# Kernel optimization log

Hardware: AMD Instinct MI355X
Metric: run time of the kernel (lower is better)

The kernel has to match this reference:

```python
import jax, jax.numpy as jnp
import numpy as np

N, C, HW, HEADS = 2048, 16, 8, 4
F = C * HW * HW  # 1024
E = 16384
EPS = 1e-5
NEG_SLOPE = 0.2


def _bn(x, g, b):
    # training-mode BatchNorm2d over (N, H, W)
    m = x.mean(axis=(0, 2, 3), keepdims=True)
    v = x.var(axis=(0, 2, 3), keepdims=True)
    return (x - m) * jax.lax.rsqrt(v + EPS) * g[None, :, None, None] + b[None, :, None, None]


def _conv1x1(x, w, b):
    # 1x1 conv == per-pixel linear: w is [out_c, in_c]
    return jnp.einsum('nchw,oc->nohw', x, w) + b[None, :, None, None]


def _gatv2(xf, edge_index, wl, bl, wr, br, att, bias_gat):
    # xf: [N, F] node features
    xl = (xf @ wl + bl).reshape(N, HEADS, F)  # source-side transform (lin_l)
    xr = (xf @ wr + br).reshape(N, HEADS, F)  # target-side transform (lin_r)
    src, dst = edge_index[0], edge_index[1]
    loops = jnp.arange(N)
    # PyG default: remove existing self loops (mask them) then add self loops
    src_f = jnp.concatenate([src, loops])
    dst_f = jnp.concatenate([dst, loops])
    valid = jnp.concatenate([src != dst, jnp.ones((N,), bool)])
    xj = xl[src_f]                                   # [E+N, HEADS, F] gather
    e = jax.nn.leaky_relu(xj + xr[dst_f], negative_slope=NEG_SLOPE)
    logits = jnp.einsum('ehf,hf->eh', e, att)        # [E+N, HEADS]
    logits = jnp.where(valid[:, None], logits, -jnp.inf)
    mx = jax.lax.stop_gradient(jax.ops.segment_max(logits, dst_f, num_segments=N))
    expv = jnp.where(valid[:, None], jnp.exp(logits - mx[dst_f]), 0.0)
    denom = jax.ops.segment_sum(expv, dst_f, num_segments=N)
    alpha = expv / denom[dst_f]                      # segment softmax over incoming edges
    out = jax.ops.segment_sum(alpha[:, :, None] * xj, dst_f, num_segments=N)  # [N, HEADS, F]
    return out.reshape(N, HEADS * F) + bias_gat


def setup_inputs() -> dict:
    key = jax.random.key(0)
    ks = jax.random.split(key, 8)
    s = 0.02
    return {
        'x': jax.random.normal(ks[0], (N, C, HW, HW), jnp.float32),
        'edge_index': jax.random.randint(ks[1], (2, E), 0, N),
        'w1': jax.random.normal(ks[2], (C, C), jnp.float32) * s,
        'b1': jnp.zeros((C,), jnp.float32),
        'g1': jnp.ones((C,), jnp.float32),
        'be1': jnp.zeros((C,), jnp.float32),
        'wl': jax.random.normal(ks[3], (F, HEADS * F), jnp.float32) * s,
        'bl': jnp.zeros((HEADS * F,), jnp.float32),
        'wr': jax.random.normal(ks[4], (F, HEADS * F), jnp.float32) * s,
        'br': jnp.zeros((HEADS * F,), jnp.float32),
        'att': jax.random.normal(ks[5], (HEADS, F), jnp.float32) * s,
        'bias_gat': jnp.zeros((HEADS * F,), jnp.float32),
        'w2': jax.random.normal(ks[6], (C, HEADS * C), jnp.float32) * s,
        'b2': jnp.zeros((C,), jnp.float32),
        'g2': jnp.ones((C,), jnp.float32),
        'be2': jnp.zeros((C,), jnp.float32),
    }


def reference(x, edge_index, w1, b1, g1, be1, wl, bl, wr, br, att, bias_gat, w2, b2, g2, be2):
    res = x
    y = _bn(_conv1x1(x, w1, b1), g1, be1)            # fc1: Conv2d 1x1 + BN
    yf = y.reshape(N, F)
    g = _gatv2(yf, edge_index, wl, bl, wr, br, att, bias_gat)
    g = g.reshape(N, HEADS * C, HW, HW)
    out = _bn(_conv1x1(g, w2, b2), g2, be2)          # fc2: Conv2d 1x1 + BN
    return out + res                                  # DropPath(0.0) == Identity
```

## Files before the change

kernel.cpp:

```cpp
#include <hip/hip_runtime.h>
#include <stdint.h>

#define N_NODES 2048
#define F_DIM   1024
#define HEADS   4
#define NF      4096
#define ROW     8192
#define E_EDGES 16384
#define MAXE    (E_EDGES + N_NODES)
#define BN_EPS  1e-5f
#define NSLOPE  0.2f

typedef unsigned short ushort_t;
typedef __attribute__((ext_vector_type(8))) short bf16x8;
typedef __attribute__((ext_vector_type(4))) float f32x4;
typedef __attribute__((ext_vector_type(8))) unsigned short us8;

__device__ __forceinline__ float b2f(unsigned short u) {
    union { unsigned int i; float f; } x; x.i = ((unsigned int)u) << 16; return x.f;
}
__device__ __forceinline__ unsigned short f2b(float f) {
    union { float f; unsigned int i; } x; x.f = f;
    unsigned int r = x.i + 0x7fffu + ((x.i >> 16) & 1u);
    return (unsigned short)(r >> 16);
}
__device__ __forceinline__ ushort_t ld_canon(const void* src, size_t i, int f32) {
    return f32 ? f2b(((const float*)src)[i]) : ((const ushort_t*)src)[i];
}
__device__ __forceinline__ float ld_f(const void* src, size_t i, int f32) {
    return f32 ? ((const float*)src)[i] : b2f(((const ushort_t*)src)[i]);
}

__device__ __forceinline__ int sniff_f32_blk(const ushort_t* xu, int* lds_flag) {
    int t = threadIdx.x;
    if (t < 64) {
        unsigned e = (xu[2 * t] >> 7) & 0xFF;
        unsigned long long m = __ballot(e >= 0x90u);
        if (t == 0) *lds_flag = (__popcll(m) >= 3) ? 1 : 0;
    }
    __syncthreads();
    return *lds_flag;
}
__device__ __forceinline__ int sniff_i64_blk(const int* ei_raw, int* lds_flag) {
    int t = threadIdx.x;
    if (t < 64) {
        unsigned long long m = __ballot(ei_raw[2 * t + 1] != 0);
        if (t == 0) *lds_flag = (m == 0ull) ? 1 : 0;
    }
    __syncthreads();
    return *lds_flag;
}

__global__ __launch_bounds__(256) void k_prep(
    const void* __restrict__ wl, const void* __restrict__ wr,
    const int* __restrict__ ei_raw, const ushort_t* __restrict__ xu,
    const void* __restrict__ x, const void* __restrict__ w1, const void* __restrict__ b1,
    ushort_t* __restrict__ wT, int* __restrict__ counts,
    ushort_t* __restrict__ y0b, float* __restrict__ ps, float* __restrict__ pq)
{
    __shared__ ushort_t tl[64][65];
    __shared__ float xs[1024];
    __shared__ float sw[256];
    __shared__ float sb[16];
    __shared__ int sfl;
    int b = blockIdx.x, t = threadIdx.x;
    if (b < 2048) {
        int f32 = sniff_f32_blk(xu, &sfl);
        int z = b >> 10, rem = b & 1023;
        int bx = (rem & 63) * 64, by = (rem >> 6) * 64;
        const void* in = z ? wr : wl;
        ushort_t* outT = wT + (size_t)z * 4194304ull;
        #pragma unroll
        for (int i = 0; i < 16; ++i) {
            int idx = t + i * 256;
            int r = idx >> 6, c = idx & 63;
            tl[r][c] = ld_canon(in, (size_t)(by + r) * 4096 + bx + c, f32);
        }
        __syncthreads();
        #pragma unroll
        for (int i = 0; i < 16; ++i) {
            int idx = t + i * 256;
            int r = idx >> 6, c = idx & 63;
            outT[(size_t)(bx + r) * 1024 + by + c] = tl[c][r];
        }
    } else if (b < 2120) {
        int i64 = sniff_i64_blk(ei_raw, &sfl);
        int idx = (b - 2048) * 256 + t;
        if (idx < E_EDGES) {
            int s = i64 ? ei_raw[2 * idx] : ei_raw[idx];
            int d = i64 ? ei_raw[2 * (E_EDGES + idx)] : ei_raw[E_EDGES + idx];
            if (s != d) atomicAdd(&counts[d], 1);
        } else if (idx < MAXE) {
            atomicAdd(&counts[idx - E_EDGES], 1);
        }
    } else {
        int bid = b - 2120;
        int f32 = sniff_f32_blk(xu, &sfl);
        sw[t] = ld_f(w1, t, f32);
        if (t < 16) sb[t] = ld_f(b1, t, f32);
        int wave = t >> 6, lane = t & 63;
        float s[4] = {0,0,0,0}, q[4] = {0,0,0,0};
        for (int nn = 0; nn < 8; ++nn) {
            int n = bid * 8 + nn;
            __syncthreads();
            #pragma unroll
            for (int i = 0; i < 4; ++i) {
                int idx = t + i * 256;
                xs[idx] = ld_f(x, (size_t)n * 1024 + idx, f32);
            }
            __syncthreads();
            #pragma unroll
            for (int i = 0; i < 4; ++i) {
                int o = wave * 4 + i;
                float acc = sb[o];
                #pragma unroll
                for (int c = 0; c < 16; ++c) acc += xs[c * 64 + lane] * sw[o * 16 + c];
                y0b[(size_t)n * 1024 + o * 64 + lane] = f2b(acc);
                s[i] += acc; q[i] += acc * acc;
            }
        }
        #pragma unroll
        for (int i = 0; i < 4; ++i)
            for (int mm = 1; mm < 64; mm <<= 1) {
                s[i] += __shfl_xor(s[i], mm);
                q[i] += __shfl_xor(q[i], mm);
            }
        if (lane == 0)
            #pragma unroll
            for (int i = 0; i < 4; ++i) {
                ps[bid * 16 + wave * 4 + i] = s[i];
                pq[bid * 16 + wave * 4 + i] = q[i];
            }
    }
}

__global__ __launch_bounds__(256) void k_scatnorm(
    const int* __restrict__ ei_raw, const int* __restrict__ counts,
    int* __restrict__ cursor, int* __restrict__ offs, int* __restrict__ esrc,
    const ushort_t* __restrict__ y0b,
    const float* __restrict__ ps, const float* __restrict__ pq,
    const void* __restrict__ g1, const void* __restrict__ be1,
    const ushort_t* __restrict__ xu, ushort_t* __restrict__ xf)
{
    __shared__ int offl[2048];
    __shared__ int ts[256];
    __shared__ int sfl;
    __shared__ float red[2][64];
    __shared__ float scs[16], shs[16];
    int t = threadIdx.x;
    if (blockIdx.x < 72) {
        int i64 = sniff_i64_blk(ei_raw, &sfl);
        int loc[8]; int tot = 0;
        #pragma unroll
        for (int j = 0; j < 8; ++j) { loc[j] = counts[t * 8 + j]; tot += loc[j]; }
        ts[t] = tot; __syncthreads();
        for (int s = 1; s < 256; s <<= 1) {
            int v = (t >= s) ? ts[t - s] : 0;
            __syncthreads();
            ts[t] += v;
            __syncthreads();
        }
        int run = ts[t] - tot;
        #pragma unroll
        for (int j = 0; j < 8; ++j) { offl[t * 8 + j] = run; run += loc[j]; }
        __syncthreads();
        if (blockIdx.x == 0) {
            #pragma unroll
            for (int j = 0; j < 8; ++j) offs[t * 8 + j] = offl[t * 8 + j];
            if (t == 255) offs[2048] = run;
        }
        int idx = blockIdx.x * 256 + t;
        if (idx < E_EDGES) {
            int s = i64 ? ei_raw[2 * idx] : ei_raw[idx];
            int d = i64 ? ei_raw[2 * (E_EDGES + idx)] : ei_raw[E_EDGES + idx];
            if (s != d) esrc[offl[d] + atomicAdd(&cursor[d], 1)] = s;
        } else if (idx < MAXE) {
            int n = idx - E_EDGES;
            esrc[offl[n] + atomicAdd(&cursor[n], 1)] = n;
        }
    } else {
        int f32 = sniff_f32_blk(xu, &sfl);
        int lane = t & 63, wv = t >> 6;
        float s = 0.f, q = 0.f;
        #pragma unroll
        for (int i = 0; i < 16; ++i) { s += ps[i * 256 + t]; q += pq[i * 256 + t]; }
        s += __shfl_xor(s, 16); q += __shfl_xor(q, 16);
        s += __shfl_xor(s, 32); q += __shfl_xor(q, 32);
        if (lane < 16) { red[0][wv * 16 + lane] = s; red[1][wv * 16 + lane] = q; }
        __syncthreads();
        if (t < 16) {
            float S = red[0][t] + red[0][16 + t] + red[0][32 + t] + red[0][48 + t];
            float Q = red[1][t] + red[1][16 + t] + red[1][32 + t] + red[1][48 + t];
            const float inv = 1.0f / 131072.0f;
            float mean = S * inv;
            float var  = Q * inv - mean * mean;
            float sc = ld_f(g1, t, f32) * rsqrtf(var + BN_EPS);
            scs[t] = sc;
            shs[t] = ld_f(be1, t, f32) - mean * sc;
        }
        __syncthreads();
        size_t base = (size_t)(blockIdx.x - 72) * 4096 + t * 16;
        int ch = ((int)(base >> 6)) & 15;
        float sc = scs[ch], sh = shs[ch];
        us8 v0 = *(const us8*)(y0b + base), v1 = *(const us8*)(y0b + base + 8);
        us8 o0, o1;
        #pragma unroll
        for (int j = 0; j < 8; ++j) {
            o0[j] = f2b(b2f(v0[j]) * sc + sh);
            o1[j] = f2b(b2f(v1[j]) * sc + sh);
        }
        *(us8*)(xf + base) = o0;
        *(us8*)(xf + base + 8) = o1;
    }
}

__global__ __launch_bounds__(256) void k_gemm(
    const ushort_t* __restrict__ A, const ushort_t* __restrict__ BT,
    const void* __restrict__ blr, const void* __restrict__ brr,
    const ushort_t* __restrict__ xu, ushort_t* __restrict__ out)
{
    __shared__ __align__(16) ushort_t smem[16384];
    ushort_t* As0 = smem;
    ushort_t* As1 = smem + 4096;
    ushort_t* Bs0 = smem + 8192;
    ushort_t* Bs1 = smem + 12288;
    ushort_t* cs  = smem;
    __shared__ int sfl;
    int f32 = sniff_f32_blk(xu, &sfl);
    int tid = threadIdx.x;
    int wv = tid >> 6, ln = tid & 63;
    int m0 = blockIdx.y * 128, n0 = blockIdx.x * 128;
    int wm = (wv >> 1) * 64, wn = (wv & 1) * 64;
    int lr = ln & 15, quad = ln >> 4;

    f32x4 acc[4][4];
    #pragma unroll
    for (int i = 0; i < 4; ++i)
        #pragma unroll
        for (int j2 = 0; j2 < 4; ++j2) acc[i][j2] = (f32x4){0.f, 0.f, 0.f, 0.f};

    for (int k0 = 0; k0 < 1024; k0 += 64) {
        #pragma unroll
        for (int i = 0; i < 2; ++i) {
            int cbase = i * 256 + wv * 64;
            int ci = cbase + ln;
            int m = ci >> 2, kc = ci & 3;
            const ushort_t* ga = A + (size_t)(m0 + m) * 1024 + k0 + kc * 8;
            __builtin_amdgcn_global_load_lds(
                (const __attribute__((address_space(1))) void*)ga,
                (__attribute__((address_space(3))) void*)(&As0[cbase * 8]), 16, 0, 0);
            __builtin_amdgcn_global_load_lds(
                (const __attribute__((address_space(1))) void*)(ga + 32),
                (__attribute__((address_space(3))) void*)(&As1[cbase * 8]), 16, 0, 0);
            const ushort_t* gb = BT + (size_t)(n0 + m) * 1024 + k0 + kc * 8;
            __builtin_amdgcn_global_load_lds(
                (const __attribute__((address_space(1))) void*)gb,
                (__attribute__((address_space(3))) void*)(&Bs0[cbase * 8]), 16, 0, 0);
            __builtin_amdgcn_global_load_lds(
                (const __attribute__((address_space(1))) void*)(gb + 32),
                (__attribute__((address_space(3))) void*)(&Bs1[cbase * 8]), 16, 0, 0);
        }
        __syncthreads();
        #pragma unroll
        for (int p = 0; p < 2; ++p) {
            const ushort_t* Ap = p ? As1 : As0;
            const ushort_t* Bp = p ? Bs1 : Bs0;
            bf16x8 af[4], bfr[4];
            #pragma unroll
            for (int i = 0; i < 4; ++i)
                af[i] = *(const bf16x8*)(&Ap[(wm + i * 16 + lr) * 32 + quad * 8]);
            #pragma unroll
            for (int j2 = 0; j2 < 4; ++j2)
                bfr[j2] = *(const bf16x8*)(&Bp[(wn + j2 * 16 + lr) * 32 + quad * 8]);
            #pragma unroll
            for (int i = 0; i < 4; ++i)
                #pragma unroll
                for (int j2 = 0; j2 < 4; ++j2)
                    acc[i][j2] = __builtin_amdgcn_mfma_f32_16x16x32_bf16(af[i], bfr[j2], acc[i][j2], 0, 0, 0);
        }
        __syncthreads();
    }
    float bj[4];
    #pragma unroll
    for (int j2 = 0; j2 < 4; ++j2) {
        int colg = n0 + wn + j2 * 16 + lr;
        bj[j2] = (colg < 4096) ? ld_f(blr, colg, f32) : ld_f(brr, colg - 4096, f32);
    }
    #pragma unroll
    for (int ph = 0; ph < 2; ++ph) {
        if ((wv >> 1) == ph) {
            #pragma unroll
            for (int i = 0; i < 4; ++i)
                #pragma unroll
                for (int j2 = 0; j2 < 4; ++j2) {
                    int col = wn + j2 * 16 + lr;
                    #pragma unroll
                    for (int r = 0; r < 4; ++r)
                        cs[(i * 16 + quad * 4 + r) * 136 + col] = f2b(acc[i][j2][r] + bj[j2]);
                }
        }
        __syncthreads();
        #pragma unroll
        for (int rr = 0; rr < 4; ++rr) {
            int slot = rr * 256 + tid;
            int row = slot >> 4, seg = slot & 15;
            us8 v = *(const us8*)&cs[row * 136 + seg * 8];
            *(us8*)(out + (size_t)(m0 + ph * 64 + row) * ROW + n0 + seg * 8) = v;
        }
        __syncthreads();
    }
}

__global__ __launch_bounds__(64) void k_gat(
    const ushort_t* __restrict__ xlr,
    const void* __restrict__ att, const void* __restrict__ bg,
    const ushort_t* __restrict__ xu,
    const int* __restrict__ offsets, const int* __restrict__ esrc,
    ushort_t* __restrict__ g)
{
    int bx = blockIdx.x;
    int d = bx >> 2, h = bx & 3;
    int l = threadIdx.x;
    int f32;
    {
        unsigned e = (xu[2 * l] >> 7) & 0xFF;
        unsigned long long m = __ballot(e >= 0x90u);
        f32 = (__popcll(m) >= 3) ? 1 : 0;
    }
    int off = offsets[d], deg = offsets[d + 1] - off;
    size_t hF = (size_t)h * F_DIM + l * 16;

    float xrv[16], attv[16];
    {
        const ushort_t* xp = xlr + ((size_t)d * ROW + NF + hF);
        us8 x0 = *(const us8*)xp, x1 = *(const us8*)(xp + 8);
        #pragma unroll
        for (int j = 0; j < 8; ++j) {
            xrv[j] = b2f(x0[j]); xrv[8 + j] = b2f(x1[j]);
            attv[j]     = ld_f(att, hF + j, f32);
            attv[8 + j] = ld_f(att, hF + 8 + j, f32);
        }
    }
    float acc[16];
    #pragma unroll
    for (int j = 0; j < 16; ++j) acc[j] = 0.f;
    float s_run = 0.f;

    for (int c0 = 0; c0 < deg; c0 += 64) {
        int cnt = min(64, deg - c0);
        int eidx = esrc[off + c0 + (l < cnt ? l : 0)];
        int e = 0;
        for (; e + 3 < cnt; e += 4) {
            int i0 = __shfl(eidx, e),     i1 = __shfl(eidx, e + 1);
            int i2 = __shfl(eidx, e + 2), i3 = __shfl(eidx, e + 3);
            const ushort_t* p0 = xlr + ((size_t)i0 * ROW + hF);
            const ushort_t* p1 = xlr + ((size_t)i1 * ROW + hF);
            const ushort_t* p2 = xlr + ((size_t)i2 * ROW + hF);
            const ushort_t* p3 = xlr + ((size_t)i3 * ROW + hF);
            us8 v0[4], v1[4];
            v0[0] = *(const us8*)p0; v1[0] = *(const us8*)(p0 + 8);
            v0[1] = *(const us8*)p1; v1[1] = *(const us8*)(p1 + 8);
            v0[2] = *(const us8*)p2; v1[2] = *(const us8*)(p2 + 8);
            v0[3] = *(const us8*)p3; v1[3] = *(const us8*)(p3 + 8);
            float tt[4];
            #pragma unroll
            for (int k = 0; k < 4; ++k) {
                float t0 = 0.f;
                #pragma unroll
                for (int j = 0; j < 8; ++j) {
                    float u;
                    u = b2f(v0[k][j]) + xrv[j];     u = u > 0.f ? u : NSLOPE * u; t0 += u * attv[j];
                    u = b2f(v1[k][j]) + xrv[8 + j]; u = u > 0.f ? u : NSLOPE * u; t0 += u * attv[8 + j];
                }
                tt[k] = t0;
            }
            #pragma unroll
            for (int mm = 1; mm < 64; mm <<= 1) {
                tt[0] += __shfl_xor(tt[0], mm);
                tt[1] += __shfl_xor(tt[1], mm);
                tt[2] += __shfl_xor(tt[2], mm);
                tt[3] += __shfl_xor(tt[3], mm);
            }
            float w0 = __expf(tt[0]), w1 = __expf(tt[1]);
            float w2v = __expf(tt[2]), w3 = __expf(tt[3]);
            s_run += w0 + w1 + w2v + w3;
            #pragma unroll
            for (int j = 0; j < 8; ++j) {
                acc[j]     += w0 * b2f(v0[0][j]) + w1 * b2f(v0[1][j])
                            + w2v * b2f(v0[2][j]) + w3 * b2f(v0[3][j]);
                acc[8 + j] += w0 * b2f(v1[0][j]) + w1 * b2f(v1[1][j])
                            + w2v * b2f(v1[2][j]) + w3 * b2f(v1[3][j]);
            }
        }
        for (; e < cnt; ++e) {
            int i0 = __shfl(eidx, e);
            const ushort_t* p = xlr + ((size_t)i0 * ROW + hF);
            us8 a0 = *(const us8*)p, a1 = *(const us8*)(p + 8);
            float t0 = 0.f;
            #pragma unroll
            for (int j = 0; j < 8; ++j) {
                float u;
                u = b2f(a0[j]) + xrv[j];     u = u > 0.f ? u : NSLOPE * u; t0 += u * attv[j];
                u = b2f(a1[j]) + xrv[8 + j]; u = u > 0.f ? u : NSLOPE * u; t0 += u * attv[8 + j];
            }
            #pragma unroll
            for (int mm = 1; mm < 64; mm <<= 1) t0 += __shfl_xor(t0, mm);
            float w0 = __expf(t0);
            s_run += w0;
            #pragma unroll
            for (int j = 0; j < 8; ++j) {
                acc[j]     += w0 * b2f(a0[j]);
                acc[8 + j] += w0 * b2f(a1[j]);
            }
        }
    }
    float inv = 1.0f / s_run;
    ushort_t* gp = g + ((size_t)d * NF + hF);
    us8 outv0, outv1;
    #pragma unroll
    for (int j = 0; j < 8; ++j) {
        outv0[j] = f2b(acc[j] * inv + ld_f(bg, hF + j, f32));
        outv1[j] = f2b(acc[8 + j] * inv + ld_f(bg, hF + 8 + j, f32));
    }
    *(us8*)gp = outv0;
    *(us8*)(gp + 8) = outv1;
}

__global__ __launch_bounds__(256) void k_fc2(
    const ushort_t* __restrict__ g, const void* __restrict__ w2, const void* __restrict__ b2,
    const ushort_t* __restrict__ xu,
    ushort_t* __restrict__ zb, float* __restrict__ ps, float* __restrict__ pq)
{
    __shared__ float gs[4096];
    __shared__ float sw[1024];
    __shared__ float sb[16];
    __shared__ int sfl;
    int f32 = sniff_f32_blk(xu, &sfl);
    int tid = threadIdx.x;
    #pragma unroll
    for (int i = 0; i < 4; ++i) sw[tid + i * 256] = ld_f(w2, tid + i * 256, f32);
    if (tid < 16) sb[tid] = ld_f(b2, tid, f32);
    int wave = tid >> 6, lane = tid & 63;
    float s[4] = {0,0,0,0}, q[4] = {0,0,0,0};
    for (int nn = 0; nn < 2; ++nn) {
        int n = blockIdx.x * 2 + nn;
        __syncthreads();
        {
            const ushort_t* gp = g + (size_t)n * 4096 + tid * 16;
            us8 v0 = *(const us8*)gp, v1 = *(const us8*)(gp + 8);
            #pragma unroll
            for (int j = 0; j < 8; ++j) {
                gs[tid * 16 + j] = b2f(v0[j]);
                gs[tid * 16 + 8 + j] = b2f(v1[j]);
            }
        }
        __syncthreads();
        float acc[4];
        #pragma unroll
        for (int i = 0; i < 4; ++i) acc[i] = sb[wave * 4 + i];
        #pragma unroll 8
        for (int k = 0; k < 64; ++k) {
            float gv = gs[k * 64 + lane];
            #pragma unroll
            for (int i = 0; i < 4; ++i)
                acc[i] += gv * sw[(wave * 4 + i) * 64 + k];
        }
        #pragma unroll
        for (int i = 0; i < 4; ++i) {
            zb[(size_t)n * 1024 + (wave * 4 + i) * 64 + lane] = f2b(acc[i]);
            s[i] += acc[i]; q[i] += acc[i] * acc[i];
        }
    }
    #pragma unroll
    for (int i = 0; i < 4; ++i)
        for (int mm = 1; mm < 64; mm <<= 1) {
            s[i] += __shfl_xor(s[i], mm);
            q[i] += __shfl_xor(q[i], mm);
        }
    if (lane == 0)
        #pragma unroll
        for (int i = 0; i < 4; ++i) {
            ps[blockIdx.x * 16 + wave * 4 + i] = s[i];
            pq[blockIdx.x * 16 + wave * 4 + i] = q[i];
        }
}

__global__ __launch_bounds__(256) void k_out(
    const ushort_t* __restrict__ zb, const void* __restrict__ x,
    const float* __restrict__ ps, const float* __restrict__ pq,
    const void* __restrict__ g2, const void* __restrict__ be2,
    void* __restrict__ out)
{
    __shared__ float red[2][64];
    __shared__ float scs[16], shs[16];
    __shared__ int sfl;
    int f32 = sniff_f32_blk((const ushort_t*)x, &sfl);
    int t = threadIdx.x, lane = t & 63, wv = t >> 6;
    float s = 0.f, q = 0.f;
    #pragma unroll
    for (int i = 0; i < 64; ++i) { s += ps[i * 256 + t]; q += pq[i * 256 + t]; }
    s += __shfl_xor(s, 16); q += __shfl_xor(q, 16);
    s += __shfl_xor(s, 32); q += __shfl_xor(q, 32);
    if (lane < 16) { red[0][wv * 16 + lane] = s; red[1][wv * 16 + lane] = q; }
    __syncthreads();
    if (t < 16) {
        float S = red[0][t] + red[0][16 + t] + red[0][32 + t] + red[0][48 + t];
        float Q = red[1][t] + red[1][16 + t] + red[1][32 + t] + red[1][48 + t];
        const float inv = 1.0f / 131072.0f;
        float mean = S * inv;
        float var  = Q * inv - mean * mean;
        float sc = ld_f(g2, t, f32) * rsqrtf(var + BN_EPS);
        scs[t] = sc;
        shs[t] = ld_f(be2, t, f32) - mean * sc;
    }
    __syncthreads();
    size_t base = (size_t)blockIdx.x * 4096;
    #pragma unroll
    for (int i = 0; i < 16; ++i) {
        size_t k = base + t + i * 256;
        int ch = ((int)k >> 6) & 15;
        float val = b2f(zb[k]) * scs[ch] + shs[ch] + ld_f(x, k, f32);
        if (f32) ((float*)out)[k] = val;
        else     ((ushort_t*)out)[k] = f2b(val);
    }
}

extern "C" void kernel_launch(void* const* d_in, const int* in_sizes, int n_in,
                              void* d_out, int out_size, void* d_ws, size_t ws_size,
                              hipStream_t stream)
{
    const void* x   = d_in[0];
    const void* ei  = d_in[1];
    const void* w1  = d_in[2];
    const void* b1  = d_in[3];
    const void* g1  = d_in[4];
    const void* be1 = d_in[5];
    const void* wl  = d_in[6];
    const void* bl  = d_in[7];
    const void* wr  = d_in[8];
    const void* br  = d_in[9];
    const void* att = d_in[10];
    const void* bg  = d_in[11];
    const void* w2  = d_in[12];
    const void* b2  = d_in[13];
    const void* g2  = d_in[14];
    const void* be2 = d_in[15];
    (void)in_sizes; (void)n_in; (void)out_size; (void)ws_size;

    char* wsb = (char*)d_ws;
    size_t o = 0;
    auto alloc = [&](size_t bytes) -> void* {
        void* p = wsb + o;
        o = (o + bytes + 255) & ~(size_t)255;
        return p;
    };
    ushort_t* y0b   = (ushort_t*)alloc(2097152ull * 2);
    ushort_t* xf    = (ushort_t*)alloc(2097152ull * 2);
    ushort_t* zb    = (ushort_t*)alloc(2097152ull * 2);
    ushort_t* wT    = (ushort_t*)alloc(8388608ull * 2);
    ushort_t* gbuf  = wT;
    ushort_t* xlr   = (ushort_t*)alloc(16777216ull * 2);
    float* p1s = (float*)alloc(256 * 16 * 4);
    float* p1q = (float*)alloc(256 * 16 * 4);
    float* p2s = (float*)alloc(1024 * 16 * 4);
    float* p2q = (float*)alloc(1024 * 16 * 4);
    int* counts = (int*)alloc(2048 * 4);
    int* cursor = (int*)alloc(2048 * 4);
    int* offs   = (int*)alloc(2049 * 4);
    int* esrc   = (int*)alloc(MAXE * 4);

    hipMemsetAsync(counts, 0, 2 * 2048 * 4, stream);
    k_prep<<<2376, 256, 0, stream>>>(wl, wr, (const int*)ei, (const ushort_t*)x,
                                     x, w1, b1, wT, counts, y0b, p1s, p1q);
    k_scatnorm<<<584, 256, 0, stream>>>((const int*)ei, counts, cursor, offs, esrc,
                                        y0b, p1s, p1q, g1, be1, (const ushort_t*)x, xf);
    k_gemm<<<dim3(64, 16), 256, 0, stream>>>(xf, wT, bl, br, (const ushort_t*)x, xlr);
    k_gat<<<N_NODES * HEADS, 64, 0, stream>>>(xlr, att, bg, (const ushort_t*)x, offs, esrc, gbuf);
    k_fc2<<<1024, 256, 0, stream>>>(gbuf, w2, b2, (const ushort_t*)x, zb, p2s, p2q);
    k_out<<<512, 256, 0, stream>>>(zb, x, p2s, p2q, g2, be2, d_out);
}
```

Baseline: 259.2 us.

## Enlarge GEMM tiles to 256x256 with 4-stage async LDS pipeline and swizzle

Rewrites the projection GEMM to use 256x256 block tiles with 8 waves, a four-deep ring of LDS stages filled by direct global-to-LDS loads, and an XOR swizzle on k-chunks to avoid bank conflicts. Loads for future k-tiles overlap MFMA work, synchronised with vmcnt waits and barriers instead of double syncthreads per step. It cuts global traffic per FLOP and barrier stalls, at the cost of 128KB LDS per block and only 256 blocks, which gives low occupancy.

```diff
diff --git a/kernel.cpp b/kernel.cpp
--- a/kernel.cpp
+++ b/kernel.cpp
@@ -214,98 +214,112 @@
     }
 }
 
-__global__ __launch_bounds__(256) void k_gemm(
+__global__ __launch_bounds__(512) void k_gemm(
     const ushort_t* __restrict__ A, const ushort_t* __restrict__ BT,
     const void* __restrict__ blr, const void* __restrict__ brr,
     const ushort_t* __restrict__ xu, ushort_t* __restrict__ out)
 {
-    __shared__ __align__(16) ushort_t smem[16384];
-    ushort_t* As0 = smem;
-    ushort_t* As1 = smem + 4096;
-    ushort_t* Bs0 = smem + 8192;
-    ushort_t* Bs1 = smem + 12288;
-    ushort_t* cs  = smem;
+    __shared__ __align__(16) ushort_t smem[65536];
     __shared__ int sfl;
     int f32 = sniff_f32_blk(xu, &sfl);
     int tid = threadIdx.x;
     int wv = tid >> 6, ln = tid & 63;
-    int m0 = blockIdx.y * 128, n0 = blockIdx.x * 128;
-    int wm = (wv >> 1) * 64, wn = (wv & 1) * 64;
+    int m0 = blockIdx.y * 256, n0 = blockIdx.x * 256;
+    int wm = (wv >> 2) * 128, wn = (wv & 3) * 64;
     int lr = ln & 15, quad = ln >> 4;
-
-    f32x4 acc[4][4];
-    #pragma unroll
-    for (int i = 0; i < 4; ++i)
-        #pragma unroll
-        for (int j2 = 0; j2 < 4; ++j2) acc[i][j2] = (f32x4){0.f, 0.f, 0.f, 0.f};
-
-    for (int k0 = 0; k0 < 1024; k0 += 64) {
-        #pragma unroll
-        for (int i = 0; i < 2; ++i) {
-            int cbase = i * 256 + wv * 64;
-            int ci = cbase + ln;
-            int m = ci >> 2, kc = ci & 3;
-            const ushort_t* ga = A + (size_t)(m0 + m) * 1024 + k0 + kc * 8;
+    int key = (lr >> 1) & 3;
+
+    f32x4 acc[8][4];
+    #pragma unroll
+    for (int i = 0; i < 8; ++i)
+        #pragma unroll
+        for (int j = 0; j < 4; ++j) acc[i][j] = (f32x4){0.f, 0.f, 0.f, 0.f};
+
+    auto stage_panel = [&](const ushort_t* G, int row0, int kt, int slot, int which) {
+        ushort_t* base = smem + which * 32768 + slot * 8192;
+        #pragma unroll
+        for (int j = 0; j < 2; ++j) {
+            int c = wv * 128 + j * 64 + ln;
+            int r = c >> 2;
+            int q = (c & 3) ^ ((r >> 1) & 3);
+            const ushort_t* g = G + (size_t)(row0 + r) * 1024 + kt * 32 + q * 8;
             __builtin_amdgcn_global_load_lds(
-                (const __attribute__((address_space(1))) void*)ga,
-                (__attribute__((address_space(3))) void*)(&As0[cbase * 8]), 16, 0, 0);
-            __builtin_amdgcn_global_load_lds(
-                (const __attribute__((address_space(1))) void*)(ga + 32),
-                (__attribute__((address_space(3))) void*)(&As1[cbase * 8]), 16, 0, 0);
-            const ushort_t* gb = BT + (size_t)(n0 + m) * 1024 + k0 + kc * 8;
-            __builtin_amdgcn_global_load_lds(
-                (const __attribute__((address_space(1))) void*)gb,
-                (__attribute__((address_space(3))) void*)(&Bs0[cbase * 8]), 16, 0, 0);
-            __builtin_amdgcn_global_load_lds(
-                (const __attribute__((address_space(1))) void*)(gb + 32),
-                (__attribute__((address_space(3))) void*)(&Bs1[cbase * 8]), 16, 0, 0);
-        }
-        __syncthreads();
-        #pragma unroll
-        for (int p = 0; p < 2; ++p) {
-            const ushort_t* Ap = p ? As1 : As0;
-            const ushort_t* Bp = p ? Bs1 : Bs0;
-            bf16x8 af[4], bfr[4];
-            #pragma unroll
-            for (int i = 0; i < 4; ++i)
-                af[i] = *(const bf16x8*)(&Ap[(wm + i * 16 + lr) * 32 + quad * 8]);
-            #pragma unroll
-            for (int j2 = 0; j2 < 4; ++j2)
-                bfr[j2] = *(const bf16x8*)(&Bp[(wn + j2 * 16 + lr) * 32 + quad * 8]);
-            #pragma unroll
-            for (int i = 0; i < 4; ++i)
+                (const __attribute__((address_space(1))) void*)g,
+                (__attribute__((address_space(3))) void*)(base + (wv * 128 + j * 64) * 8),
+                16, 0, 0);
+        }
+    };
+
+    auto compute_tile = [&](int t) {
+        const ushort_t* Ab = smem + (t & 3) * 8192;
+        const ushort_t* Bb = smem + 32768 + (t & 3) * 8192;
+        bf16x8 bfrag[4];
+        #pragma unroll
+        for (int j = 0; j < 4; ++j) {
+            int col = wn + j * 16 + lr;
+            bfrag[j] = *(const bf16x8*)(Bb + col * 32 + ((quad ^ key) * 8));
+        }
+        #pragma unroll
+        for (int i = 0; i < 8; ++i) {
+            int row = wm + i * 16 + lr;
+            bf16x8 af = *(const bf16x8*)(Ab + row * 32 + ((quad ^ key) * 8));
+            #pragma unroll
+            for (int j = 0; j < 4; ++j)
+                acc[i][j] = __builtin_amdgcn_mfma_f32_16x16x32_bf16(af, bfrag[j], acc[i][j], 0, 0, 0);
+        }
+    };
+
+    stage_panel(A, m0, 0, 0, 0); stage_panel(BT, n0, 0, 0, 1);
+    stage_panel(A, m0, 1, 1, 0); stage_panel(BT, n0, 1, 1, 1);
+    stage_panel(A, m0, 2, 2, 0); stage_panel(BT, n0, 2, 2, 1);
+
+    #pragma unroll 1
+    for (int t = 0; t < 29; ++t) {
+        asm volatile("s_waitcnt vmcnt(8)" ::: "memory");
+        __builtin_amdgcn_s_barrier();
+        int tn = t + 3;
+        stage_panel(A, m0, tn, tn & 3, 0);
+        stage_panel(BT, n0, tn, tn & 3, 1);
+        compute_tile(t);
+    }
+    asm volatile("s_waitcnt vmcnt(8)" ::: "memory");
+    __builtin_amdgcn_s_barrier();
+    compute_tile(29);
+    asm volatile("s_waitcnt vmcnt(4)" ::: "memory");
+    __builtin_amdgcn_s_barrier();
+    compute_tile(30);
+    asm volatile("s_waitcnt vmcnt(0)" ::: "memory");
+    __builtin_amdgcn_s_barrier();
+    compute_tile(31);
+
+    __syncthreads();
+    float bj[4];
+    #pragma unroll
+    for (int j = 0; j < 4; ++j) {
+        int colg = n0 + wn + j * 16 + lr;
+        bj[j] = (colg < 4096) ? ld_f(blr, colg, f32) : ld_f(brr, colg - 4096, f32);
+    }
+    ushort_t* cs = smem;
+    #pragma unroll
+    for (int ph = 0; ph < 2; ++ph) {
+        if ((wv >> 2) == ph) {
+            #pragma unroll
+            for (int i = 0; i < 8; ++i)
                 #pragma unroll
-                for (int j2 = 0; j2 < 4; ++j2)
-                    acc[i][j2] = __builtin_amdgcn_mfma_f32_16x16x32_bf16(af[i], bfr[j2], acc[i][j2], 0, 0, 0);
-        }
-        __syncthreads();
-    }
-    float bj[4];
-    #pragma unroll
-    for (int j2 = 0; j2 < 4; ++j2) {
-        int colg = n0 + wn + j2 * 16 + lr;
-        bj[j2] = (colg < 4096) ? ld_f(blr, colg, f32) : ld_f(brr, colg - 4096, f32);
-    }
-    #pragma unroll
-    for (int ph = 0; ph < 2; ++ph) {
-        if ((wv >> 1) == ph) {
-            #pragma unroll
-            for (int i = 0; i < 4; ++i)
-                #pragma unroll
-                for (int j2 = 0; j2 < 4; ++j2) {
-                    int col = wn + j2 * 16 + lr;
+                for (int j = 0; j < 4; ++j) {
+                    int col = wn + j * 16 + lr;
                     #pragma unroll
                     for (int r = 0; r < 4; ++r)
-                        cs[(i * 16 + quad * 4 + r) * 136 + col] = f2b(acc[i][j2][r] + bj[j2]);
+                        cs[(i * 16 + quad * 4 + r) * 264 + col] = f2b(acc[i][j][r] + bj[j]);
                 }
         }
         __syncthreads();
         #pragma unroll
-        for (int rr = 0; rr < 4; ++rr) {
-            int slot = rr * 256 + tid;
-            int row = slot >> 4, seg = slot & 15;
-            us8 v = *(const us8*)&cs[row * 136 + seg * 8];
-            *(us8*)(out + (size_t)(m0 + ph * 64 + row) * ROW + n0 + seg * 8) = v;
+        for (int rr = 0; rr < 8; ++rr) {
+            int slot = rr * 512 + tid;
+            int row = slot >> 5, seg = slot & 31;
+            us8 v = *(const us8*)&cs[row * 264 + seg * 8];
+            *(us8*)(out + (size_t)(m0 + ph * 128 + row) * ROW + n0 + seg * 8) = v;
         }
         __syncthreads();
     }
@@ -574,7 +588,7 @@
                                      x, w1, b1, wT, counts, y0b, p1s, p1q);
     k_scatnorm<<<584, 256, 0, stream>>>((const int*)ei, counts, cursor, offs, esrc,
                                         y0b, p1s, p1q, g1, be1, (const ushort_t*)x, xf);
-    k_gemm<<<dim3(64, 16), 256, 0, stream>>>(xf, wT, bl, br, (const ushort_t*)x, xlr);
+    k_gemm<<<dim3(32, 8), 512, 0, stream>>>(xf, wT, bl, br, (const ushort_t*)x, xlr);
     k_gat<<<N_NODES * HEADS, 64, 0, stream>>>(xlr, att, bg, (const ushort_t*)x, offs, esrc, gbuf);
     k_fc2<<<1024, 256, 0, stream>>>(gbuf, w2, b2, (const ushort_t*)x, zb, p2s, p2q);
     k_out<<<512, 256, 0, stream>>>(zb, x, p2s, p2q, g2, be2, d_out);
```

Result: no change. 261.7 us (+0.9%).
